# Optimization experiments

Hardware: AMD Instinct MI355X
Metric: run time of the kernel (lower is better)

## Reference

```python
import jax, jax.numpy as jnp
import numpy as np

N_NODES = 50000
N_EDGES = 800000


def gcn_layer(h_in, W, b, src, dst, n_nodes):
    """PyG GCNConv: linear transform, add self-loops, symmetric-normalized scatter-add."""
    h = h_in @ W  # [N, out]
    loop = jnp.arange(n_nodes, dtype=src.dtype)
    s = jnp.concatenate([src, loop])  # [E+N]
    d = jnp.concatenate([dst, loop])  # [E+N]
    deg = jax.ops.segment_sum(jnp.ones_like(d, dtype=h.dtype), d, num_segments=n_nodes)
    dinv = jnp.where(deg > 0, jax.lax.rsqrt(deg), 0.0)  # deg^{-1/2}
    norm = dinv[s] * dinv[d]  # [E+N]
    msg = h[s] * norm[:, None]  # gather + scale, [E+N, out]
    out = jax.ops.segment_sum(msg, d, num_segments=n_nodes)  # scatter-add
    return out + b


def setup_inputs() -> dict:
    key = jax.random.key(0)
    ks = jax.random.split(key, 8)
    Din, H1, H2, Dout = 128, 128, 128, 64
    x = jax.random.normal(ks[0], (N_NODES, Din), dtype=jnp.float32)
    edge_index = jax.random.randint(ks[1], (2, N_EDGES), 0, N_NODES, dtype=jnp.int64)
    # Glorot-ish init for weights
    W1 = jax.random.normal(ks[2], (Din, H1), dtype=jnp.float32) / np.sqrt(Din)
    W2 = jax.random.normal(ks[3], (H1, H2), dtype=jnp.float32) / np.sqrt(H1)
    W3 = jax.random.normal(ks[4], (H2, Dout), dtype=jnp.float32) / np.sqrt(H2)
    b1 = jnp.zeros((H1,), dtype=jnp.float32)
    b2 = jnp.zeros((H2,), dtype=jnp.float32)
    b3 = jnp.zeros((Dout,), dtype=jnp.float32)
    return {"x": x, "edge_index": edge_index, "W1": W1, "b1": b1,
            "W2": W2, "b2": b2, "W3": W3, "b3": b3}


def reference(x, edge_index, W1, b1, W2, b2, W3, b3):
    src, dst = edge_index[0], edge_index[1]
    n = x.shape[0]
    h = gcn_layer(x, W1, b1, src, dst, n)
    h = jax.nn.relu(h)  # dropout p=0 -> identity
    h = gcn_layer(h, W2, b2, src, dst, n)
    h = jax.nn.relu(h)
    h = gcn_layer(h, W3, b3, src, dst, n)
    return h
```

## Files before the change

### kernel.cpp

```cpp
#include <hip/hip_runtime.h>
#include <hip/hip_fp16.h>

#define N_NODES 50000
#define N_EDGES 800000
#define CEILDIV(a,b) (((a)+(b)-1)/(b))
#define NB_SCAN CEILDIV(N_NODES, 256)

__global__ __launch_bounds__(256) void k_deg_count(const int* __restrict__ dst,
                                                   int* __restrict__ degcnt, int e) {
    int i = blockIdx.x * 256 + threadIdx.x;
    if (i < e) atomicAdd(&degcnt[dst[i]], 1);
}

__global__ __launch_bounds__(256) void k_blocksum(const int* __restrict__ degcnt,
                                                  int* __restrict__ bsum, int n) {
    __shared__ int part[256];
    const int tid = threadIdx.x;
    const int gid = blockIdx.x * 256 + tid;
    part[tid] = (gid < n) ? degcnt[gid] : 0;
    __syncthreads();
    for (int off = 128; off > 0; off >>= 1) {
        if (tid < off) part[tid] += part[tid + off];
        __syncthreads();
    }
    if (tid == 0) bsum[blockIdx.x] = part[0];
}

__global__ __launch_bounds__(256) void k_scanb(const int* __restrict__ bsum,
                                               int* __restrict__ boff) {
    __shared__ int part[256];
    const int tid = threadIdx.x;
    part[tid] = (tid < NB_SCAN) ? bsum[tid] : 0;
    __syncthreads();
    for (int off = 1; off < 256; off <<= 1) {
        int v = (tid >= off) ? part[tid - off] : 0;
        __syncthreads();
        part[tid] += v;
        __syncthreads();
    }
    if (tid < NB_SCAN) boff[tid] = (tid == 0) ? 0 : part[tid - 1];
}

__global__ __launch_bounds__(256) void k_rowstart(const int* __restrict__ degcnt,
                                                  const int* __restrict__ boff,
                                                  int* __restrict__ rowstart,
                                                  float* __restrict__ dinv, int n) {
    __shared__ int part[256];
    const int tid = threadIdx.x;
    const int gid = blockIdx.x * 256 + tid;
    const int d = (gid < n) ? degcnt[gid] : 0;
    part[tid] = d;
    __syncthreads();
    for (int off = 1; off < 256; off <<= 1) {
        int v = (tid >= off) ? part[tid - off] : 0;
        __syncthreads();
        part[tid] += v;
        __syncthreads();
    }
    if (gid < n) {
        rowstart[gid] = boff[blockIdx.x] + part[tid] - d;
        dinv[gid] = rsqrtf((float)(d + 1));
    }
    if (gid == 0) rowstart[n] = N_EDGES;
}

__global__ __launch_bounds__(256) void k_bin(const int* __restrict__ src,
                                             const int* __restrict__ dst,
                                             const int* __restrict__ rowstart,
                                             int* __restrict__ cursor,
                                             int* __restrict__ esrc, int e) {
    int i = blockIdx.x * 256 + threadIdx.x;
    if (i < e) {
        int d = dst[i];
        int pos = rowstart[d] + atomicAdd(&cursor[d], 1);
        esrc[pos] = src[i];
    }
}

template<int K, bool RELU>
__global__ __launch_bounds__(256) void k_gemm(const float* __restrict__ A,
                                              const float* __restrict__ W,
                                              const float* __restrict__ dinv,
                                              __half* __restrict__ C, int n) {
    constexpr int CG   = K / 4;
    constexpr int RG   = 256 / CG;
    constexpr int ROWS = RG * 4;
    __shared__ float4 Wl4[128 * CG];

    const int tid  = threadIdx.x;
    const int row0 = blockIdx.x * ROWS;

    constexpr int WV = (128 * CG) / 256;
    const float4* W4 = (const float4*)W;
#pragma unroll
    for (int i = 0; i < WV; ++i) Wl4[tid + i * 256] = W4[tid + i * 256];
    __syncthreads();

    const int cg = tid % CG;
    const int rg = tid / CG;
    const int gr = row0 + rg * 4;

    const float4* p0 = (const float4*)A + (size_t)min(gr + 0, n - 1) * 32;
    const float4* p1 = (const float4*)A + (size_t)min(gr + 1, n - 1) * 32;
    const float4* p2 = (const float4*)A + (size_t)min(gr + 2, n - 1) * 32;
    const float4* p3 = (const float4*)A + (size_t)min(gr + 3, n - 1) * 32;

    float4 acc0 = make_float4(0.f, 0.f, 0.f, 0.f);
    float4 acc1 = acc0, acc2 = acc0, acc3 = acc0;

#pragma unroll 2
    for (int m4 = 0; m4 < 32; ++m4) {
        float4 a0 = p0[m4], a1 = p1[m4], a2 = p2[m4], a3 = p3[m4];
        if (RELU) {
            a0.x = fmaxf(a0.x, 0.f); a0.y = fmaxf(a0.y, 0.f); a0.z = fmaxf(a0.z, 0.f); a0.w = fmaxf(a0.w, 0.f);
            a1.x = fmaxf(a1.x, 0.f); a1.y = fmaxf(a1.y, 0.f); a1.z = fmaxf(a1.z, 0.f); a1.w = fmaxf(a1.w, 0.f);
            a2.x = fmaxf(a2.x, 0.f); a2.y = fmaxf(a2.y, 0.f); a2.z = fmaxf(a2.z, 0.f); a2.w = fmaxf(a2.w, 0.f);
            a3.x = fmaxf(a3.x, 0.f); a3.y = fmaxf(a3.y, 0.f); a3.z = fmaxf(a3.z, 0.f); a3.w = fmaxf(a3.w, 0.f);
        }
        const float4 w0 = Wl4[(m4 * 4 + 0) * CG + cg];
        const float4 w1 = Wl4[(m4 * 4 + 1) * CG + cg];
        const float4 w2 = Wl4[(m4 * 4 + 2) * CG + cg];
        const float4 w3 = Wl4[(m4 * 4 + 3) * CG + cg];

#define ROW_STEP(A_, ACC_)                                    \
        {                                                     \
            ACC_.x = fmaf(A_.x, w0.x, ACC_.x);                \
            ACC_.x = fmaf(A_.y, w1.x, ACC_.x);                \
            ACC_.x = fmaf(A_.z, w2.x, ACC_.x);                \
            ACC_.x = fmaf(A_.w, w3.x, ACC_.x);                \
            ACC_.y = fmaf(A_.x, w0.y, ACC_.y);                \
            ACC_.y = fmaf(A_.y, w1.y, ACC_.y);                \
            ACC_.y = fmaf(A_.z, w2.y, ACC_.y);                \
            ACC_.y = fmaf(A_.w, w3.y, ACC_.y);                \
            ACC_.z = fmaf(A_.x, w0.z, ACC_.z);                \
            ACC_.z = fmaf(A_.y, w1.z, ACC_.z);                \
            ACC_.z = fmaf(A_.z, w2.z, ACC_.z);                \
            ACC_.z = fmaf(A_.w, w3.z, ACC_.z);                \
            ACC_.w = fmaf(A_.x, w0.w, ACC_.w);                \
            ACC_.w = fmaf(A_.y, w1.w, ACC_.w);                \
            ACC_.w = fmaf(A_.z, w2.w, ACC_.w);                \
            ACC_.w = fmaf(A_.w, w3.w, ACC_.w);                \
        }
        ROW_STEP(a0, acc0);
        ROW_STEP(a1, acc1);
        ROW_STEP(a2, acc2);
        ROW_STEP(a3, acc3);
#undef ROW_STEP
    }

    {
        float d0 = dinv[min(gr + 0, n - 1)];
        float d1 = dinv[min(gr + 1, n - 1)];
        float d2 = dinv[min(gr + 2, n - 1)];
        float d3 = dinv[min(gr + 3, n - 1)];
        union { __half2 h2[2]; uint2 u; } pk0, pk1, pk2, pk3;
        pk0.h2[0] = __floats2half2_rn(acc0.x * d0, acc0.y * d0);
        pk0.h2[1] = __floats2half2_rn(acc0.z * d0, acc0.w * d0);
        pk1.h2[0] = __floats2half2_rn(acc1.x * d1, acc1.y * d1);
        pk1.h2[1] = __floats2half2_rn(acc1.z * d1, acc1.w * d1);
        pk2.h2[0] = __floats2half2_rn(acc2.x * d2, acc2.y * d2);
        pk2.h2[1] = __floats2half2_rn(acc2.z * d2, acc2.w * d2);
        pk3.h2[0] = __floats2half2_rn(acc3.x * d3, acc3.y * d3);
        pk3.h2[1] = __floats2half2_rn(acc3.z * d3, acc3.w * d3);
        if (gr + 0 < n) ((uint2*)C)[(size_t)(gr + 0) * CG + cg] = pk0.u;
        if (gr + 1 < n) ((uint2*)C)[(size_t)(gr + 1) * CG + cg] = pk1.u;
        if (gr + 2 < n) ((uint2*)C)[(size_t)(gr + 2) * CG + cg] = pk2.u;
        if (gr + 3 < n) ((uint2*)C)[(size_t)(gr + 3) * CG + cg] = pk3.u;
    }
}

template<int K>
__global__ __launch_bounds__(256) void k_aggregate(const __half* __restrict__ h,
                                                   const int* __restrict__ rowstart,
                                                   const int* __restrict__ esrc,
                                                   const float* __restrict__ dinv,
                                                   const float* __restrict__ b,
                                                   float* __restrict__ out, int n) {
    constexpr int VEC = K / 32;
    const int tid  = threadIdx.x;
    const int l5   = tid & 31;
    const int base = tid & 32;
    const int node = blockIdx.x * 8 + (tid >> 5);
    if (node >= n) return;

    float a0, a1, a2 = 0.f, a3 = 0.f;
    if (VEC == 4) {
        uint2 raw = ((const uint2*)h)[(size_t)node * 32 + l5];
        union { uint2 u; __half2 h2[2]; } c; c.u = raw;
        float2 lo = __half22float2(c.h2[0]);
        float2 hi = __half22float2(c.h2[1]);
        a0 = lo.x; a1 = lo.y; a2 = hi.x; a3 = hi.y;
    } else {
        uint raw = ((const uint*)h)[(size_t)node * 32 + l5];
        union { uint u; __half2 h2; } c; c.u = raw;
        float2 lo = __half22float2(c.h2);
        a0 = lo.x; a1 = lo.y;
    }

    int row = rowstart[node];
    const int end = rowstart[node + 1];

#define GATHER(SRC_, OK_)                                                     \
    if (VEC == 4) {                                                           \
        uint2 raw = make_uint2(0u, 0u);                                       \
        if (OK_) raw = ((const uint2*)h)[(size_t)(SRC_) * 32 + l5];           \
        union { uint2 u; __half2 h2[2]; } c; c.u = raw;                       \
        float2 lo = __half22float2(c.h2[0]);                                  \
        float2 hi = __half22float2(c.h2[1]);                                  \
        a0 += lo.x; a1 += lo.y; a2 += hi.x; a3 += hi.y;                       \
    } else {                                                                  \
        uint raw = 0u;                                                        \
        if (OK_) raw = ((const uint*)h)[(size_t)(SRC_) * 32 + l5];            \
        union { uint u; __half2 h2; } c; c.u = raw;                           \
        float2 lo = __half22float2(c.h2);                                     \
        a0 += lo.x; a1 += lo.y;                                               \
    }

    while (row < end) {
        int cnt = end - row;
        if (cnt > 32) cnt = 32;
        int s_l = (l5 < cnt) ? esrc[row + l5] : 0;
        for (int jj = 0; jj < cnt; jj += 8) {
            const int i0 = jj + 0, i1 = jj + 1, i2 = jj + 2, i3 = jj + 3;
            const int i4 = jj + 4, i5 = jj + 5, i6 = jj + 6, i7 = jj + 7;
            const int s0 = __shfl(s_l, base + i0);
            const int s1 = __shfl(s_l, base + i1);
            const int s2 = __shfl(s_l, base + i2);
            const int s3 = __shfl(s_l, base + i3);
            const int s4 = __shfl(s_l, base + i4);
            const int s5 = __shfl(s_l, base + i5);
            const int s6 = __shfl(s_l, base + i6);
            const int s7 = __shfl(s_l, base + i7);
            GATHER(s0, i0 < cnt);
            GATHER(s1, i1 < cnt);
            GATHER(s2, i2 < cnt);
            GATHER(s3, i3 < cnt);
            GATHER(s4, i4 < cnt);
            GATHER(s5, i5 < cnt);
            GATHER(s6, i6 < cnt);
            GATHER(s7, i7 < cnt);
        }
        row += cnt;
    }
#undef GATHER

    const float dd = dinv[node];
    if (VEC == 4) {
        float4 bb = ((const float4*)b)[l5];
        float4 o;
        o.x = a0 * dd + bb.x;
        o.y = a1 * dd + bb.y;
        o.z = a2 * dd + bb.z;
        o.w = a3 * dd + bb.w;
        ((float4*)out)[(size_t)node * 32 + l5] = o;
    } else {
        float2 bb = ((const float2*)b)[l5];
        float2 o;
        o.x = a0 * dd + bb.x;
        o.y = a1 * dd + bb.y;
        ((float2*)out)[(size_t)node * 32 + l5] = o;
    }
}

extern "C" void kernel_launch(void* const* d_in, const int* in_sizes, int n_in,
                              void* d_out, int out_size, void* d_ws, size_t ws_size,
                              hipStream_t stream) {
    const float* x  = (const float*)d_in[0];
    const int*   ei = (const int*)d_in[1];
    const float* W1 = (const float*)d_in[2];
    const float* b1 = (const float*)d_in[3];
    const float* W2 = (const float*)d_in[4];
    const float* b2 = (const float*)d_in[5];
    const float* W3 = (const float*)d_in[6];
    const float* b3 = (const float*)d_in[7];
    float* out = (float*)d_out;

    const int* src = ei;
    const int* dst = ei + N_EDGES;

    char* ws = (char*)d_ws;
    size_t off = 0;
    auto alloc = [&](size_t bytes) {
        void* p = ws + off;
        off += (bytes + 255) & ~(size_t)255;
        return p;
    };
    int*    degcnt   = (int*)alloc((size_t)N_NODES * 2 * 4);
    int*    cursor   = degcnt + N_NODES;
    int*    rowstart = (int*)alloc((N_NODES + 1) * 4);
    float*  dinv     = (float*)alloc(N_NODES * 4);
    int*    bsum     = (int*)alloc(NB_SCAN * 4);
    int*    boff     = (int*)alloc(NB_SCAN * 4);
    int*    esrc     = (int*)alloc((size_t)N_EDGES * 4);
    __half* hbuf     = (__half*)alloc((size_t)N_NODES * 128 * 2);
    float*  abuf     = (float*)alloc((size_t)N_NODES * 128 * 4);

    const int n = N_NODES, e = N_EDGES;

    hipMemsetAsync(degcnt, 0, (size_t)N_NODES * 2 * 4, stream);
    k_deg_count<<<CEILDIV(e, 256), 256, 0, stream>>>(dst, degcnt, e);
    k_blocksum<<<NB_SCAN, 256, 0, stream>>>(degcnt, bsum, n);
    k_scanb<<<1, 256, 0, stream>>>(bsum, boff);
    k_rowstart<<<NB_SCAN, 256, 0, stream>>>(degcnt, boff, rowstart, dinv, n);
    k_bin<<<CEILDIV(e, 256), 256, 0, stream>>>(src, dst, rowstart, cursor, esrc, e);

    k_gemm<128, false><<<CEILDIV(n, 32), 256, 0, stream>>>(x, W1, dinv, hbuf, n);
    k_aggregate<128><<<CEILDIV(n, 8), 256, 0, stream>>>(hbuf, rowstart, esrc, dinv, b1, abuf, n);

    k_gemm<128, true><<<CEILDIV(n, 32), 256, 0, stream>>>(abuf, W2, dinv, hbuf, n);
    k_aggregate<128><<<CEILDIV(n, 8), 256, 0, stream>>>(hbuf, rowstart, esrc, dinv, b2, abuf, n);

    k_gemm<64, true><<<CEILDIV(n, 64), 256, 0, stream>>>(abuf, W3, dinv, hbuf, n);
    k_aggregate<64><<<CEILDIV(n, 8), 256, 0, stream>>>(hbuf, rowstart, esrc, dinv, b3, out, n);
}
```

Measured before the change: 344.9 us.

## Use fp16 MFMA GEMMs with half-precision intermediate activations

Replaces the FP32 FMA GEMM with an fp16 MFMA 16x16x32 kernel. A and transposed W tiles are staged in swizzled LDS, and ReLU is applied by bit-masking negative halves. Inputs and weights are converted to fp16 by new pre-pass kernels, and the hidden aggregation outputs are stored as fp16, which halves activation traffic. This adds conversion launches and per-element half stores, and it lowers precision of intermediate activations.

```diff
diff --git a/kernel.cpp b/kernel.cpp
--- a/kernel.cpp
+++ b/kernel.cpp
@@ -5,6 +5,9 @@
 #define N_EDGES 800000
 #define CEILDIV(a,b) (((a)+(b)-1)/(b))
 #define NB_SCAN CEILDIV(N_NODES, 256)
+
+typedef _Float16 half8 __attribute__((ext_vector_type(8)));
+typedef float    f32x4 __attribute__((ext_vector_type(4)));
 
 __global__ __launch_bounds__(256) void k_deg_count(const int* __restrict__ dst,
                                                    int* __restrict__ degcnt, int e) {
@@ -77,105 +80,116 @@
     }
 }
 
-template<int K, bool RELU>
-__global__ __launch_bounds__(256) void k_gemm(const float* __restrict__ A,
-                                              const float* __restrict__ W,
+__global__ __launch_bounds__(256) void k_x2h(const float* __restrict__ x,
+                                             __half* __restrict__ xh, long total) {
+    long i = (long)(blockIdx.x * 256 + threadIdx.x) * 8;
+    if (i >= total) return;
+    float4 lo = ((const float4*)x)[i / 4];
+    float4 hi = ((const float4*)x)[i / 4 + 1];
+    union { __half2 h2[4]; uint4 u; } pk;
+    pk.h2[0] = __floats2half2_rn(lo.x, lo.y);
+    pk.h2[1] = __floats2half2_rn(lo.z, lo.w);
+    pk.h2[2] = __floats2half2_rn(hi.x, hi.y);
+    pk.h2[3] = __floats2half2_rn(hi.z, hi.w);
+    ((uint4*)xh)[i / 8] = pk.u;
+}
+
+template<int KOUT>
+__global__ __launch_bounds__(256) void k_w2h(const float* __restrict__ W,
+                                             __half* __restrict__ Wt) {
+    int idx = blockIdx.x * 256 + threadIdx.x;
+    if (idx >= KOUT * 128) return;
+    int c = idx >> 7;
+    int k = idx & 127;
+    Wt[c * 128 + k] = __float2half(W[(size_t)k * KOUT + c]);
+}
+
+template<int KOUT, bool RELU>
+__global__ __launch_bounds__(256) void k_gemm(const __half* __restrict__ A,
+                                              const __half* __restrict__ Wt,
                                               const float* __restrict__ dinv,
                                               __half* __restrict__ C, int n) {
-    constexpr int CG   = K / 4;
-    constexpr int RG   = 256 / CG;
-    constexpr int ROWS = RG * 4;
-    __shared__ float4 Wl4[128 * CG];
+    constexpr int NT     = KOUT / 16;
+    constexpr int ABYTES = 64 * 256;
+    constexpr int WBYTES = KOUT * 256;
+    __shared__ uint4 ldsbuf[(ABYTES + WBYTES) / 16];
+    char* Als = (char*)ldsbuf;
+    char* Wls = Als + ABYTES;
 
     const int tid  = threadIdx.x;
-    const int row0 = blockIdx.x * ROWS;
-
-    constexpr int WV = (128 * CG) / 256;
-    const float4* W4 = (const float4*)W;
-#pragma unroll
-    for (int i = 0; i < WV; ++i) Wl4[tid + i * 256] = W4[tid + i * 256];
+    const int row0 = blockIdx.x * 64;
+
+#pragma unroll
+    for (int i = 0; i < 4; ++i) {
+        int g   = tid + i * 256;
+        int r   = g >> 4;
+        int ch  = g & 15;
+        int gr  = row0 + r;
+        uint4 v = make_uint4(0u, 0u, 0u, 0u);
+        if (gr < n) v = ((const uint4*)A)[(size_t)gr * 16 + ch];
+        if (RELU) {
+            uint n0 = (v.x >> 15) & 0x00010001u; v.x &= ~(n0 * 0xFFFFu);
+            uint n1 = (v.y >> 15) & 0x00010001u; v.y &= ~(n1 * 0xFFFFu);
+            uint n2 = (v.z >> 15) & 0x00010001u; v.z &= ~(n2 * 0xFFFFu);
+            uint n3 = (v.w >> 15) & 0x00010001u; v.w &= ~(n3 * 0xFFFFu);
+        }
+        *(uint4*)(Als + r * 256 + ((ch * 16) ^ ((r & 7) << 4))) = v;
+    }
+#pragma unroll
+    for (int i = 0; i < WBYTES / 16 / 256; ++i) {
+        int g  = tid + i * 256;
+        int r  = g >> 4;
+        int ch = g & 15;
+        uint4 v = ((const uint4*)Wt)[(size_t)r * 16 + ch];
+        *(uint4*)(Wls + r * 256 + ((ch * 16) ^ ((r & 7) << 4))) = v;
+    }
     __syncthreads();
 
-    const int cg = tid % CG;
-    const int rg = tid / CG;
-    const int gr = row0 + rg * 4;
-
-    const float4* p0 = (const float4*)A + (size_t)min(gr + 0, n - 1) * 32;
-    const float4* p1 = (const float4*)A + (size_t)min(gr + 1, n - 1) * 32;
-    const float4* p2 = (const float4*)A + (size_t)min(gr + 2, n - 1) * 32;
-    const float4* p3 = (const float4*)A + (size_t)min(gr + 3, n - 1) * 32;
-
-    float4 acc0 = make_float4(0.f, 0.f, 0.f, 0.f);
-    float4 acc1 = acc0, acc2 = acc0, acc3 = acc0;
-
-#pragma unroll 2
-    for (int m4 = 0; m4 < 32; ++m4) {
-        float4 a0 = p0[m4], a1 = p1[m4], a2 = p2[m4], a3 = p3[m4];
-        if (RELU) {
-            a0.x = fmaxf(a0.x, 0.f); a0.y = fmaxf(a0.y, 0.f); a0.z = fmaxf(a0.z, 0.f); a0.w = fmaxf(a0.w, 0.f);
-            a1.x = fmaxf(a1.x, 0.f); a1.y = fmaxf(a1.y, 0.f); a1.z = fmaxf(a1.z, 0.f); a1.w = fmaxf(a1.w, 0.f);
-            a2.x = fmaxf(a2.x, 0.f); a2.y = fmaxf(a2.y, 0.f); a2.z = fmaxf(a2.z, 0.f); a2.w = fmaxf(a2.w, 0.f);
-            a3.x = fmaxf(a3.x, 0.f); a3.y = fmaxf(a3.y, 0.f); a3.z = fmaxf(a3.z, 0.f); a3.w = fmaxf(a3.w, 0.f);
-        }
-        const float4 w0 = Wl4[(m4 * 4 + 0) * CG + cg];
-        const float4 w1 = Wl4[(m4 * 4 + 1) * CG + cg];
-        const float4 w2 = Wl4[(m4 * 4 + 2) * CG + cg];
-        const float4 w3 = Wl4[(m4 * 4 + 3) * CG + cg];
-
-#define ROW_STEP(A_, ACC_)                                    \
-        {                                                     \
-            ACC_.x = fmaf(A_.x, w0.x, ACC_.x);                \
-            ACC_.x = fmaf(A_.y, w1.x, ACC_.x);                \
-            ACC_.x = fmaf(A_.z, w2.x, ACC_.x);                \
-            ACC_.x = fmaf(A_.w, w3.x, ACC_.x);                \
-            ACC_.y = fmaf(A_.x, w0.y, ACC_.y);                \
-            ACC_.y = fmaf(A_.y, w1.y, ACC_.y);                \
-            ACC_.y = fmaf(A_.z, w2.y, ACC_.y);                \
-            ACC_.y = fmaf(A_.w, w3.y, ACC_.y);                \
-            ACC_.z = fmaf(A_.x, w0.z, ACC_.z);                \
-            ACC_.z = fmaf(A_.y, w1.z, ACC_.z);                \
-            ACC_.z = fmaf(A_.z, w2.z, ACC_.z);                \
-            ACC_.z = fmaf(A_.w, w3.z, ACC_.z);                \
-            ACC_.w = fmaf(A_.x, w0.w, ACC_.w);                \
-            ACC_.w = fmaf(A_.y, w1.w, ACC_.w);                \
-            ACC_.w = fmaf(A_.z, w2.w, ACC_.w);                \
-            ACC_.w = fmaf(A_.w, w3.w, ACC_.w);                \
-        }
-        ROW_STEP(a0, acc0);
-        ROW_STEP(a1, acc1);
-        ROW_STEP(a2, acc2);
-        ROW_STEP(a3, acc3);
-#undef ROW_STEP
-    }
-
-    {
-        float d0 = dinv[min(gr + 0, n - 1)];
-        float d1 = dinv[min(gr + 1, n - 1)];
-        float d2 = dinv[min(gr + 2, n - 1)];
-        float d3 = dinv[min(gr + 3, n - 1)];
-        union { __half2 h2[2]; uint2 u; } pk0, pk1, pk2, pk3;
-        pk0.h2[0] = __floats2half2_rn(acc0.x * d0, acc0.y * d0);
-        pk0.h2[1] = __floats2half2_rn(acc0.z * d0, acc0.w * d0);
-        pk1.h2[0] = __floats2half2_rn(acc1.x * d1, acc1.y * d1);
-        pk1.h2[1] = __floats2half2_rn(acc1.z * d1, acc1.w * d1);
-        pk2.h2[0] = __floats2half2_rn(acc2.x * d2, acc2.y * d2);
-        pk2.h2[1] = __floats2half2_rn(acc2.z * d2, acc2.w * d2);
-        pk3.h2[0] = __floats2half2_rn(acc3.x * d3, acc3.y * d3);
-        pk3.h2[1] = __floats2half2_rn(acc3.z * d3, acc3.w * d3);
-        if (gr + 0 < n) ((uint2*)C)[(size_t)(gr + 0) * CG + cg] = pk0.u;
-        if (gr + 1 < n) ((uint2*)C)[(size_t)(gr + 1) * CG + cg] = pk1.u;
-        if (gr + 2 < n) ((uint2*)C)[(size_t)(gr + 2) * CG + cg] = pk2.u;
-        if (gr + 3 < n) ((uint2*)C)[(size_t)(gr + 3) * CG + cg] = pk3.u;
-    }
-}
-
-template<int K>
+    const int wave = tid >> 6;
+    const int lane = tid & 63;
+    const int l15  = lane & 15;
+    const int l4   = lane >> 4;
+
+    f32x4 acc[NT];
+#pragma unroll
+    for (int ct = 0; ct < NT; ++ct) acc[ct] = (f32x4){0.f, 0.f, 0.f, 0.f};
+
+#pragma unroll
+    for (int kb = 0; kb < 4; ++kb) {
+        const int arow = 16 * wave + l15;
+        half8 af = *(half8*)(Als + arow * 256 +
+                             (((kb * 64) + l4 * 16) ^ ((arow & 7) << 4)));
+#pragma unroll
+        for (int ct = 0; ct < NT; ++ct) {
+            const int wrow = ct * 16 + l15;
+            half8 bf = *(half8*)(Wls + wrow * 256 +
+                                 (((kb * 64) + l4 * 16) ^ ((wrow & 7) << 4)));
+            acc[ct] = __builtin_amdgcn_mfma_f32_16x16x32_f16(af, bf, acc[ct], 0, 0, 0);
+        }
+    }
+
+    const int rbase = row0 + 16 * wave + l4 * 4;
+    const float d0 = dinv[min(rbase + 0, n - 1)];
+    const float d1 = dinv[min(rbase + 1, n - 1)];
+    const float d2 = dinv[min(rbase + 2, n - 1)];
+    const float d3 = dinv[min(rbase + 3, n - 1)];
+#pragma unroll
+    for (int ct = 0; ct < NT; ++ct) {
+        const int col = ct * 16 + l15;
+        if (rbase + 0 < n) C[(size_t)(rbase + 0) * KOUT + col] = __float2half(acc[ct][0] * d0);
+        if (rbase + 1 < n) C[(size_t)(rbase + 1) * KOUT + col] = __float2half(acc[ct][1] * d1);
+        if (rbase + 2 < n) C[(size_t)(rbase + 2) * KOUT + col] = __float2half(acc[ct][2] * d2);
+        if (rbase + 3 < n) C[(size_t)(rbase + 3) * KOUT + col] = __float2half(acc[ct][3] * d3);
+    }
+}
+
+template<int K, bool HOUT>
 __global__ __launch_bounds__(256) void k_aggregate(const __half* __restrict__ h,
                                                    const int* __restrict__ rowstart,
                                                    const int* __restrict__ esrc,
                                                    const float* __restrict__ dinv,
                                                    const float* __restrict__ b,
-                                                   float* __restrict__ out, int n) {
+                                                   void* __restrict__ out, int n) {
     constexpr int VEC = K / 32;
     const int tid  = threadIdx.x;
     const int l5   = tid & 31;
@@ -247,18 +261,26 @@
     const float dd = dinv[node];
     if (VEC == 4) {
         float4 bb = ((const float4*)b)[l5];
-        float4 o;
-        o.x = a0 * dd + bb.x;
-        o.y = a1 * dd + bb.y;
-        o.z = a2 * dd + bb.z;
-        o.w = a3 * dd + bb.w;
-        ((float4*)out)[(size_t)node * 32 + l5] = o;
+        float o0 = a0 * dd + bb.x, o1 = a1 * dd + bb.y;
+        float o2 = a2 * dd + bb.z, o3 = a3 * dd + bb.w;
+        if (HOUT) {
+            union { __half2 h2[2]; uint2 u; } pk;
+            pk.h2[0] = __floats2half2_rn(o0, o1);
+            pk.h2[1] = __floats2half2_rn(o2, o3);
+            ((uint2*)out)[(size_t)node * 32 + l5] = pk.u;
+        } else {
+            ((float4*)out)[(size_t)node * 32 + l5] = make_float4(o0, o1, o2, o3);
+        }
     } else {
         float2 bb = ((const float2*)b)[l5];
-        float2 o;
-        o.x = a0 * dd + bb.x;
-        o.y = a1 * dd + bb.y;
-        ((float2*)out)[(size_t)node * 32 + l5] = o;
+        float o0 = a0 * dd + bb.x, o1 = a1 * dd + bb.y;
+        if (HOUT) {
+            union { __half2 h2; uint u; } pk;
+            pk.h2 = __floats2half2_rn(o0, o1);
+            ((uint*)out)[(size_t)node * 32 + l5] = pk.u;
+        } else {
+            ((float2*)out)[(size_t)node * 32 + l5] = make_float2(o0, o1);
+        }
     }
 }
 
@@ -292,8 +314,12 @@
     int*    bsum     = (int*)alloc(NB_SCAN * 4);
     int*    boff     = (int*)alloc(NB_SCAN * 4);
     int*    esrc     = (int*)alloc((size_t)N_EDGES * 4);
+    __half* xh       = (__half*)alloc((size_t)N_NODES * 128 * 2);
     __half* hbuf     = (__half*)alloc((size_t)N_NODES * 128 * 2);
-    float*  abuf     = (float*)alloc((size_t)N_NODES * 128 * 4);
+    __half* abuf     = (__half*)alloc((size_t)N_NODES * 128 * 2);
+    __half* wt1      = (__half*)alloc(128 * 128 * 2);
+    __half* wt2      = (__half*)alloc(128 * 128 * 2);
+    __half* wt3      = (__half*)alloc(64 * 128 * 2);
 
     const int n = N_NODES, e = N_EDGES;
 
@@ -304,12 +330,17 @@
     k_rowstart<<<NB_SCAN, 256, 0, stream>>>(degcnt, boff, rowstart, dinv, n);
     k_bin<<<CEILDIV(e, 256), 256, 0, stream>>>(src, dst, rowstart, cursor, esrc, e);
 
-    k_gemm<128, false><<<CEILDIV(n, 32), 256, 0, stream>>>(x, W1, dinv, hbuf, n);
-    k_aggregate<128><<<CEILDIV(n, 8), 256, 0, stream>>>(hbuf, rowstart, esrc, dinv, b1, abuf, n);
-
-    k_gemm<128, true><<<CEILDIV(n, 32), 256, 0, stream>>>(abuf, W2, dinv, hbuf, n);
-    k_aggregate<128><<<CEILDIV(n, 8), 256, 0, stream>>>(hbuf, rowstart, esrc, dinv, b2, abuf, n);
-
-    k_gemm<64, true><<<CEILDIV(n, 64), 256, 0, stream>>>(abuf, W3, dinv, hbuf, n);
-    k_aggregate<64><<<CEILDIV(n, 8), 256, 0, stream>>>(hbuf, rowstart, esrc, dinv, b3, out, n);
-}
+    k_x2h<<<CEILDIV((long)n * 128, 8 * 256), 256, 0, stream>>>(x, xh, (long)n * 128);
+    k_w2h<128><<<CEILDIV(128 * 128, 256), 256, 0, stream>>>(W1, wt1);
+    k_w2h<128><<<CEILDIV(128 * 128, 256), 256, 0, stream>>>(W2, wt2);
+    k_w2h<64><<<CEILDIV(64 * 128, 256), 256, 0, stream>>>(W3, wt3);
+
+    k_gemm<128, false><<<CEILDIV(n, 64), 256, 0, stream>>>(xh, wt1, dinv, hbuf, n);
+    k_aggregate<128, true><<<CEILDIV(n, 8), 256, 0, stream>>>(hbuf, rowstart, esrc, dinv, b1, abuf, n);
+
+    k_gemm<128, true><<<CEILDIV(n, 64), 256, 0, stream>>>(abuf, wt2, dinv, hbuf, n);
+    k_aggregate<128, true><<<CEILDIV(n, 8), 256, 0, stream>>>(hbuf, rowstart, esrc, dinv, b2, abuf, n);
+
+    k_gemm<64, true><<<CEILDIV(n, 64), 256, 0, stream>>>(abuf, wt3, dinv, hbuf, n);
+    k_aggregate<64, false><<<CEILDIV(n, 8), 256, 0, stream>>>(hbuf, rowstart, esrc, dinv, b3, out, n);
+}
```

Result: faster. 291.9 us (-15.4%).
